# Kernel tuning notes

Measured on AMD Instinct MI355X. Metric: run time of the kernel, lower is better.

Reference implementation:

```python
import jax, jax.numpy as jnp
import numpy as np

N_NODES = 50000
N_EDGES = 600000
F_IN = 64
N_GRAPHS = 2000
OUT_DIM = 1
BN_EPS = 1e-5


def _bn(x, gamma, beta):
    # BatchNorm1d training-mode forward: biased batch stats over node/row dim
    m = jnp.mean(x, axis=0)
    v = jnp.var(x, axis=0)
    return (x - m) * jax.lax.rsqrt(v + BN_EPS) * gamma + beta


def _gcn(x, W, b, src, dst):
    # PyG GCNConv: h = x @ W; symmetric-normalized aggregation with self-loops; bias after agg
    n = x.shape[0]
    h = x @ W                                    # [N, C_out]
    ones = jnp.ones((src.shape[0],), h.dtype)
    deg = jax.ops.segment_sum(ones, dst, num_segments=n) + 1.0  # +1 self-loop
    dinv = jax.lax.rsqrt(deg)
    norm = (dinv[src] * dinv[dst])[:, None]      # [E, 1]
    agg = jax.ops.segment_sum(h[src] * norm, dst, num_segments=n)
    agg = agg + h * (1.0 / deg)[:, None]         # self-loop term: deg^{-1/2}*deg^{-1/2}
    return agg + b


def _pool_mean(x, batch, g):
    s = jax.ops.segment_sum(x, batch, num_segments=g)
    c = jax.ops.segment_sum(jnp.ones((x.shape[0],), x.dtype), batch, num_segments=g)
    return s / jnp.maximum(c, 1.0)[:, None]


def _forward(xc, xs, W1c, b1c, g1c, be1c, W2c, b2c, g2c, be2c,
             W1s, b1s, g1s, be1s, W2s, b2s, g2s, be2s,
             Wf1, bf1, gf1, bef1, Wf2, bf2,
             src_c, dst_c, src_s, dst_s, batch):
    hc = jax.nn.relu(_bn(_gcn(xc, W1c, b1c, src_c, dst_c), g1c, be1c))
    hc = jax.nn.relu(_bn(_gcn(hc, W2c, b2c, src_c, dst_c), g2c, be2c))
    hs = jax.nn.relu(_bn(_gcn(xs, W1s, b1s, src_s, dst_s), g1s, be1s))
    hs = jax.nn.relu(_bn(_gcn(hs, W2s, b2s, src_s, dst_s), g2s, be2s))
    pc = _pool_mean(hc, batch, N_GRAPHS)         # [G, 64]
    ps = _pool_mean(hs, batch, N_GRAPHS)         # [G, 64]
    h = jnp.concatenate([pc, ps], axis=1)        # [G, 128]
    h = jax.nn.relu(_bn(h @ Wf1 + bf1, gf1, bef1))  # dropout is identity in eval
    return h @ Wf2 + bf2                         # [G, OUT_DIM]


def setup_inputs() -> dict:
    key = jax.random.key(0)
    ks = jax.random.split(key, 16)

    def glorot(k, fan_in, fan_out):
        s = np.sqrt(2.0 / (fan_in + fan_out)).astype(np.float32)
        return jax.random.normal(k, (fan_in, fan_out), jnp.float32) * s

    inp = {
        'x_chromophore': jax.random.normal(ks[0], (N_NODES, F_IN), jnp.float32),
        'x_solvent': jax.random.normal(ks[1], (N_NODES, F_IN), jnp.float32),
        'edge_index_chromophore': jax.random.randint(ks[2], (2, N_EDGES), 0, N_NODES),
        'edge_index_solvent': jax.random.randint(ks[3], (2, N_EDGES), 0, N_NODES),
        'batch': jnp.sort(jax.random.randint(ks[4], (N_NODES,), 0, N_GRAPHS)),
        # chromophore branch params
        'W1c': glorot(ks[5], F_IN, 128), 'b1c': jnp.zeros((128,), jnp.float32),
        'g1c': jnp.ones((128,), jnp.float32), 'be1c': jnp.zeros((128,), jnp.float32),
        'W2c': glorot(ks[6], 128, 64), 'b2c': jnp.zeros((64,), jnp.float32),
        'g2c': jnp.ones((64,), jnp.float32), 'be2c': jnp.zeros((64,), jnp.float32),
        # solvent branch params
        'W1s': glorot(ks[7], F_IN, 128), 'b1s': jnp.zeros((128,), jnp.float32),
        'g1s': jnp.ones((128,), jnp.float32), 'be1s': jnp.zeros((128,), jnp.float32),
        'W2s': glorot(ks[8], 128, 64), 'b2s': jnp.zeros((64,), jnp.float32),
        'g2s': jnp.ones((64,), jnp.float32), 'be2s': jnp.zeros((64,), jnp.float32),
        # MLP head
        'Wf1': glorot(ks[9], 128, 64), 'bf1': jnp.zeros((64,), jnp.float32),
        'gf1': jnp.ones((64,), jnp.float32), 'bef1': jnp.zeros((64,), jnp.float32),
        'Wf2': glorot(ks[10], 64, OUT_DIM), 'bf2': jnp.zeros((OUT_DIM,), jnp.float32),
    }
    return inp


def reference(x_chromophore, x_solvent, edge_index_chromophore, edge_index_solvent, batch,
              W1c, b1c, g1c, be1c, W2c, b2c, g2c, be2c,
              W1s, b1s, g1s, be1s, W2s, b2s, g2s, be2s,
              Wf1, bf1, gf1, bef1, Wf2, bf2):
    src_c, dst_c = edge_index_chromophore[0], edge_index_chromophore[1]
    src_s, dst_s = edge_index_solvent[0], edge_index_solvent[1]
    return _forward(x_chromophore, x_solvent,
                    W1c, b1c, g1c, be1c, W2c, b2c, g2c, be2c,
                    W1s, b1s, g1s, be1s, W2s, b2s, g2s, be2s,
                    Wf1, bf1, gf1, bef1, Wf2, bf2,
                    src_c, dst_c, src_s, dst_s, batch)
```

## Files before the change

### kernel.cpp

```cpp
#include <hip/hip_runtime.h>
#include <hip/hip_bf16.h>
#include <cstdint>
#include <cstddef>

#define NN 50000
#define NE 600000
#define NG 2000
#define NBUCK 49
#define SLOTS 16
#define NCHUNK 3125
#define PNE (NE + NBUCK * 15 * 1024)

typedef __attribute__((ext_vector_type(8))) short bf8;
typedef __attribute__((ext_vector_type(4))) float f32x4;

__device__ __forceinline__ unsigned short f2bf(float f) {
    uint32_t u = __float_as_uint(f);
    uint32_t r = (u + 0x7FFFu + ((u >> 16) & 1u)) >> 16;
    return (unsigned short)r;
}
__device__ __forceinline__ float bf2f(unsigned short h) {
    return __uint_as_float(((uint32_t)h) << 16);
}
__device__ __forceinline__ float lo16(uint32_t v) { return __uint_as_float(v << 16); }
__device__ __forceinline__ float hi16(uint32_t v) { return __uint_as_float(v & 0xFFFF0000u); }

__global__ __launch_bounds__(256) void conv_bf16_kernel(const float* __restrict__ x0,
                                                        const float* __restrict__ x1,
                                                        unsigned short* __restrict__ out) {
    int b = blockIdx.y;
    const float* x = b ? x1 : x0;
    unsigned short* o = out + (size_t)b * NN * 64;
    int i = (blockIdx.x * 256 + threadIdx.x) * 4;
    if (i + 3 < NN * 64) {
        float4 v = *(const float4*)&x[i];
        ushort4 r = make_ushort4(f2bf(v.x), f2bf(v.y), f2bf(v.z), f2bf(v.w));
        *(ushort4*)&o[i] = r;
    }
}

template<int K, int N>
__global__ __launch_bounds__(256) void pack_w(const float* __restrict__ W0,
                                              const float* __restrict__ W1,
                                              unsigned short* __restrict__ out) {
    int b = blockIdx.y;
    const float* W = b ? W1 : W0;
    unsigned short* o = out + (size_t)b * K * N;
    int idx = blockIdx.x * 256 + threadIdx.x;
    const int total = (N / 16) * (K / 32) * 64;
    if (idx >= total) return;
    int l = idx & 63;
    int th = idx >> 6;
    int h = th % (K / 32);
    int t = th / (K / 32);
    int col = t * 16 + (l & 15);
    int k0 = h * 32 + (l >> 4) * 8;
    ushort4 lo = make_ushort4(f2bf(W[(k0 + 0) * N + col]), f2bf(W[(k0 + 1) * N + col]),
                              f2bf(W[(k0 + 2) * N + col]), f2bf(W[(k0 + 3) * N + col]));
    ushort4 hi = make_ushort4(f2bf(W[(k0 + 4) * N + col]), f2bf(W[(k0 + 5) * N + col]),
                              f2bf(W[(k0 + 6) * N + col]), f2bf(W[(k0 + 7) * N + col]));
    *(ushort4*)&o[idx * 8] = lo;
    *(ushort4*)&o[idx * 8 + 4] = hi;
}

__global__ __launch_bounds__(256) void bucket_hist(const int* __restrict__ d0,
                                                   const int* __restrict__ d1,
                                                   int* __restrict__ bucketCnt, int nE) {
    int b = blockIdx.y;
    const int* dst = b ? d1 : d0;
    __shared__ int h[NBUCK];
    for (int i = threadIdx.x; i < NBUCK; i += 256) h[i] = 0;
    __syncthreads();
    for (int e = blockIdx.x * 256 + threadIdx.x; e < nE; e += gridDim.x * 256)
        atomicAdd(&h[dst[e] >> 10], 1);
    __syncthreads();
    for (int i = threadIdx.x; i < NBUCK; i += 256)
        if (h[i]) atomicAdd(&bucketCnt[b * NBUCK + i], h[i]);
}

__global__ void bucket_scan(const int* __restrict__ bucketCnt,
                            int* __restrict__ bucketOff, int* __restrict__ bucketCur) {
    int b = threadIdx.x;
    if (b < 2) {
        int run = 0;
        for (int i = 0; i < NBUCK; ++i) {
            bucketOff[b * NBUCK + i] = run;
            bucketCur[b * NBUCK + i] = run;
            run += bucketCnt[b * NBUCK + i];
        }
    }
}

__global__ __launch_bounds__(256) void bucket_scatter(const int* __restrict__ s0,
                                                      const int* __restrict__ d0,
                                                      const int* __restrict__ s1,
                                                      const int* __restrict__ d1,
                                                      int* __restrict__ bucketCur,
                                                      uint32_t* __restrict__ bent, int nE) {
    int b = blockIdx.y;
    const int* src = b ? s1 : s0;
    const int* dst = b ? d1 : d0;
    __shared__ int cnt[NBUCK];
    __shared__ int base[NBUCK];
    const int tid = threadIdx.x;
    for (int i = tid; i < NBUCK; i += 256) cnt[i] = 0;
    __syncthreads();

    const int e0 = blockIdx.x * 2048 + tid;
    int bk[8], slot[8];
    uint32_t pay[8];
#pragma unroll
    for (int k = 0; k < 8; ++k) {
        int e = e0 + k * 256;
        if (e < nE) {
            int d = dst[e], s = src[e];
            bk[k] = d >> 10;
            pay[k] = ((uint32_t)(d & 1023) << 16) | (uint32_t)s;
            slot[k] = atomicAdd(&cnt[bk[k]], 1);
        } else bk[k] = -1;
    }
    __syncthreads();
    for (int i = tid; i < NBUCK; i += 256) {
        int c = cnt[i];
        base[i] = c ? atomicAdd(&bucketCur[b * NBUCK + i], c) : 0;
    }
    __syncthreads();
#pragma unroll
    for (int k = 0; k < 8; ++k)
        if (bk[k] >= 0)
            bent[(size_t)b * (size_t)PNE + base[bk[k]] + slot[k]] = pay[k];
}

__global__ __launch_bounds__(256) void csr_build(const uint32_t* __restrict__ bent,
                                                 const int* __restrict__ bucketOff,
                                                 const int* __restrict__ bucketCnt,
                                                 int2* __restrict__ rpe,
                                                 float* __restrict__ dinv,
                                                 uint16_t* __restrict__ perm) {
    __shared__ int lcnt[1024];
    __shared__ int lcur[1024];
    __shared__ int sscan[256];
    const int bk = blockIdx.x;
    const int b = blockIdx.y;
    const int tid = threadIdx.x;
    const int ebase = bucketOff[b * NBUCK + bk];
    const int ecnt = bucketCnt[b * NBUCK + bk];
    const int P0 = ebase + bk * 15360;
    const int node0 = bk << 10;
    const uint32_t* be = bent + (size_t)b * (size_t)PNE + ebase;
    int2* rp = rpe + (size_t)b * NN;
    float* dv = dinv + (size_t)b * NN;
    uint16_t* pm = perm + (size_t)b * (size_t)PNE + P0;

    for (int i = tid; i < 1024; i += 256) lcnt[i] = 0;
    __syncthreads();
    for (int i = tid; i < ecnt; i += 256) atomicAdd(&lcnt[be[i] >> 16], 1);
    __syncthreads();

    int c[4], pc[4], s = 0;
#pragma unroll
    for (int j = 0; j < 4; ++j) {
        c[j] = lcnt[tid * 4 + j];
        pc[j] = (c[j] + 15) & ~15;
        s += pc[j];
    }
    sscan[tid] = s;
    __syncthreads();
    for (int off = 1; off < 256; off <<= 1) {
        int v = (tid >= off) ? sscan[tid - off] : 0;
        __syncthreads();
        sscan[tid] += v;
        __syncthreads();
    }
    int run = sscan[tid] - s;
#pragma unroll
    for (int j = 0; j < 4; ++j) {
        int nl = tid * 4 + j;
        int g = node0 + nl;
        if (g < NN) {
            rp[g] = make_int2(P0 + run, P0 + run + pc[j]);
            lcur[nl] = run;
            dv[g] = rsqrtf((float)c[j] + 1.0f);
        }
        run += pc[j];
    }
    __syncthreads();

    for (int i = tid; i < ecnt; i += 256) {
        uint32_t en = be[i];
        int nl = en >> 16;
        int pos = atomicAdd(&lcur[nl], 1);
        pm[pos] = (uint16_t)(en & 0xFFFFu);
    }
    __syncthreads();

    int run2 = sscan[tid] - s;
#pragma unroll
    for (int j = 0; j < 4; ++j) {
        int g = node0 + tid * 4 + j;
        if (g < NN)
            for (int t = c[j]; t < pc[j]; ++t) pm[run2 + t] = 0xFFFFu;
        run2 += pc[j];
    }
}

__global__ __launch_bounds__(256) void weight_fill(const uint16_t* __restrict__ perm,
                                                   const float* __restrict__ dinv,
                                                   uint32_t* __restrict__ permw, int nE) {
    int b = blockIdx.y;
    const uint16_t* pm = perm + (size_t)b * (size_t)PNE;
    const float* dv = dinv + (size_t)b * NN;
    uint32_t* pw = permw + (size_t)b * (size_t)PNE;
    int i = (blockIdx.x * 256 + threadIdx.x) * 4;
    if (i + 3 < nE) {
        ushort4 s4 = *(const ushort4*)&pm[i];
        uint4 o;
        o.x = (s4.x < NN) ? (((uint32_t)f2bf(dv[s4.x]) << 16) | (uint32_t)s4.x) : 0u;
        o.y = (s4.y < NN) ? (((uint32_t)f2bf(dv[s4.y]) << 16) | (uint32_t)s4.y) : 0u;
        o.z = (s4.z < NN) ? (((uint32_t)f2bf(dv[s4.z]) << 16) | (uint32_t)s4.z) : 0u;
        o.w = (s4.w < NN) ? (((uint32_t)f2bf(dv[s4.w]) << 16) | (uint32_t)s4.w) : 0u;
        *(uint4*)&pw[i] = o;
    } else {
        for (; i < nE; ++i) {
            uint16_t s = pm[i];
            pw[i] = (s < NN) ? (((uint32_t)f2bf(dv[s]) << 16) | (uint32_t)s) : 0u;
        }
    }
}

__global__ __launch_bounds__(256) void gemm1_mfma(const unsigned short* __restrict__ Xbf,
                                                  const unsigned short* __restrict__ Wp,
                                                  unsigned short* __restrict__ Y) {
    const int b = blockIdx.y;
    const unsigned short* __restrict__ X = Xbf + (size_t)b * NN * 64;
    const unsigned short* __restrict__ W = Wp + (size_t)b * 64 * 128;
    unsigned short* __restrict__ Yb = Y + (size_t)b * NN * 128;
    const int tid = threadIdx.x;
    const int w = tid >> 6, lane = tid & 63;
    const int chunk = blockIdx.x * 4 + w;
    if (chunk >= NCHUNK) return;
    const int m = lane & 15, quad = lane >> 4;

    const int row = chunk * 16 + m;
    bf8 a0 = *(const bf8*)&X[(size_t)row * 64 + quad * 8];
    bf8 a1 = *(const bf8*)&X[(size_t)row * 64 + 32 + quad * 8];
    f32x4 acc[8];
#pragma unroll
    for (int t = 0; t < 8; ++t) acc[t] = (f32x4){0.f, 0.f, 0.f, 0.f};
#pragma unroll
    for (int t = 0; t < 8; ++t) {
        bf8 b0 = *(const bf8*)&W[((t * 2 + 0) * 64 + lane) * 8];
        bf8 b1 = *(const bf8*)&W[((t * 2 + 1) * 64 + lane) * 8];
        acc[t] = __builtin_amdgcn_mfma_f32_16x16x32_bf16(b0, a0, acc[t], 0, 0, 0);
        acc[t] = __builtin_amdgcn_mfma_f32_16x16x32_bf16(b1, a1, acc[t], 0, 0, 0);
    }
#pragma unroll
    for (int t = 0; t < 8; ++t) {
        uint32_t lo = (uint32_t)f2bf(acc[t][0]) | ((uint32_t)f2bf(acc[t][1]) << 16);
        uint32_t hi = (uint32_t)f2bf(acc[t][2]) | ((uint32_t)f2bf(acc[t][3]) << 16);
        *(uint2*)&Yb[(size_t)row * 128 + t * 16 + quad * 4] = make_uint2(lo, hi);
    }
}

__global__ __launch_bounds__(256) void stats128_bf16(const unsigned short* __restrict__ Y,
                                                     float* __restrict__ sums) {
    const int b = blockIdx.y;
    const unsigned short* __restrict__ Yb = Y + (size_t)b * NN * 128;
    const int g = threadIdx.x & 31;
    const int rs = threadIdx.x >> 5;
    float s0 = 0.f, s1 = 0.f, s2 = 0.f, s3 = 0.f;
    float q0 = 0.f, q1 = 0.f, q2 = 0.f, q3 = 0.f;
    for (int r = blockIdx.x * 8 + rs; r < NN; r += gridDim.x * 8) {
        uint2 v = *(const uint2*)&Yb[(size_t)r * 128 + g * 4];
        float x0 = lo16(v.x);
        float x1 = hi16(v.x);
        float x2 = lo16(v.y);
        float x3 = hi16(v.y);
        s0 += x0; s1 += x1; s2 += x2; s3 += x3;
        q0 = fmaf(x0, x0, q0); q1 = fmaf(x1, x1, q1);
        q2 = fmaf(x2, x2, q2); q3 = fmaf(x3, x3, q3);
    }
    __shared__ float ls[8][128], lq[8][128];
    *(float4*)&ls[rs][g * 4] = make_float4(s0, s1, s2, s3);
    *(float4*)&lq[rs][g * 4] = make_float4(q0, q1, q2, q3);
    __syncthreads();
    if (threadIdx.x < 128) {
        const int c = threadIdx.x;
        float S = 0.f, Q = 0.f;
#pragma unroll
        for (int k = 0; k < 8; ++k) { S += ls[k][c]; Q += lq[k][c]; }
        int slot = blockIdx.x & (SLOTS - 1);
        float* sb = sums + (size_t)(b * SLOTS + slot) * 256;
        atomicAdd(&sb[c], S);
        atomicAdd(&sb[128 + c], Q);
    }
}

__global__ __launch_bounds__(256) void gemm2_mfma(const unsigned short* __restrict__ H1,
                                                  const unsigned short* __restrict__ Wp,
                                                  const float* __restrict__ sums,
                                                  const float* __restrict__ g0,
                                                  const float* __restrict__ g1,
                                                  const float* __restrict__ be0,
                                                  const float* __restrict__ be1,
                                                  unsigned short* __restrict__ Y) {
    __shared__ float scLds[128], shLds[128];
    const int b = blockIdx.y;
    const unsigned short* __restrict__ X = H1 + (size_t)b * NN * 128;
    const unsigned short* __restrict__ W = Wp + (size_t)b * 128 * 64;
    unsigned short* __restrict__ Yb = Y + (size_t)b * NN * 64;
    const int tid = threadIdx.x;

    if (tid < 128) {
        float s = 0.f, s2 = 0.f;
#pragma unroll
        for (int k = 0; k < SLOTS; ++k) {
            const float* sb = sums + (size_t)(b * SLOTS + k) * 256;
            s += sb[tid];
            s2 += sb[128 + tid];
        }
        const float invN = 1.0f / (float)NN;
        float mean = s * invN;
        float var = s2 * invN - mean * mean;
        float gamma = b ? g1[tid] : g0[tid];
        float beta = b ? be1[tid] : be0[tid];
        float sc = gamma * rsqrtf(var + 1e-5f);
        scLds[tid] = sc;
        shLds[tid] = beta - mean * sc;
    }
    __syncthreads();

    const int w = tid >> 6, lane = tid & 63;
    const int chunk = blockIdx.x * 4 + w;
    if (chunk >= NCHUNK) return;
    const int m = lane & 15, quad = lane >> 4;
    const int row = chunk * 16 + m;

    f32x4 acc[4];
#pragma unroll
    for (int t = 0; t < 4; ++t) acc[t] = (f32x4){0.f, 0.f, 0.f, 0.f};
#pragma unroll
    for (int h = 0; h < 4; ++h) {
        const int k0 = h * 32 + quad * 8;
        bf8 araw = *(const bf8*)&X[(size_t)row * 128 + k0];
        float4 sc0 = *(const float4*)&scLds[k0];
        float4 sc1 = *(const float4*)&scLds[k0 + 4];
        float4 sh0 = *(const float4*)&shLds[k0];
        float4 sh1 = *(const float4*)&shLds[k0 + 4];
        float scv[8] = {sc0.x, sc0.y, sc0.z, sc0.w, sc1.x, sc1.y, sc1.z, sc1.w};
        float shv[8] = {sh0.x, sh0.y, sh0.z, sh0.w, sh1.x, sh1.y, sh1.z, sh1.w};
        bf8 af;
#pragma unroll
        for (int j = 0; j < 8; ++j) {
            float v = bf2f((unsigned short)araw[j]);
            v = fmaxf(fmaf(v, scv[j], shv[j]), 0.f);
            af[j] = (short)f2bf(v);
        }
#pragma unroll
        for (int t = 0; t < 4; ++t) {
            bf8 bf = *(const bf8*)&W[((t * 4 + h) * 64 + lane) * 8];
            acc[t] = __builtin_amdgcn_mfma_f32_16x16x32_bf16(bf, af, acc[t], 0, 0, 0);
        }
    }
#pragma unroll
    for (int t = 0; t < 4; ++t) {
        uint32_t lo = (uint32_t)f2bf(acc[t][0]) | ((uint32_t)f2bf(acc[t][1]) << 16);
        uint32_t hi = (uint32_t)f2bf(acc[t][2]) | ((uint32_t)f2bf(acc[t][3]) << 16);
        *(uint2*)&Yb[(size_t)row * 64 + t * 16 + quad * 4] = make_uint2(lo, hi);
    }
}

template<bool STATS>
__global__ __launch_bounds__(256) void agg2_kernel(const unsigned short* __restrict__ hall,
                                                   const int2* __restrict__ rpe,
                                                   const uint32_t* __restrict__ permw,
                                                   const float* __restrict__ dinv,
                                                   unsigned short* __restrict__ out,
                                                   float* __restrict__ sums, int nNodes) {
    const int b = blockIdx.y;
    const unsigned short* __restrict__ h = hall + (size_t)b * NN * 64;
    const int2* rp = rpe + (size_t)b * NN;
    const uint32_t* pe = permw + (size_t)b * (size_t)PNE;
    const float* dv = dinv + (size_t)b * NN;
    unsigned short* ob = out + (size_t)b * nNodes * 64;

    const int w = threadIdx.x >> 6;
    const int wave = blockIdx.x * 4 + w;
    const int lane = threadIdx.x & 63;
    const int g = lane >> 3;
    const int c = lane & 7;
    float a0 = 0.f, a1 = 0.f, a2 = 0.f, a3 = 0.f;
    float a4 = 0.f, a5 = 0.f, a6 = 0.f, a7 = 0.f;
    float fv[8];
#pragma unroll
    for (int j = 0; j < 8; ++j) fv[j] = 0.f;

    const bool active = wave < nNodes;
    if (active) {
        const int d = wave;
        const float di = dv[d];
        const int2 pr = rp[d];
        for (int p = pr.x; p < pr.y; p += 16) {
            const uint32_t e0 = pe[p + g];
            const uint32_t e1 = pe[p + 8 + g];
            const int i0 = (int)(e0 & 0xFFFFu);
            const int i1 = (int)(e1 & 0xFFFFu);
            const float w0 = __uint_as_float(e0 & 0xFFFF0000u);
            const float w1 = __uint_as_float(e1 & 0xFFFF0000u);
            const uint4 v0 = *(const uint4*)&h[(size_t)i0 * 64 + c * 8];
            const uint4 v1 = *(const uint4*)&h[(size_t)i1 * 64 + c * 8];
            a0 = fmaf(w0, lo16(v0.x), a0); a1 = fmaf(w0, hi16(v0.x), a1);
            a2 = fmaf(w0, lo16(v0.y), a2); a3 = fmaf(w0, hi16(v0.y), a3);
            a4 = fmaf(w0, lo16(v0.z), a4); a5 = fmaf(w0, hi16(v0.z), a5);
            a6 = fmaf(w0, lo16(v0.w), a6); a7 = fmaf(w0, hi16(v0.w), a7);
            a0 = fmaf(w1, lo16(v1.x), a0); a1 = fmaf(w1, hi16(v1.x), a1);
            a2 = fmaf(w1, lo16(v1.y), a2); a3 = fmaf(w1, hi16(v1.y), a3);
            a4 = fmaf(w1, lo16(v1.z), a4); a5 = fmaf(w1, hi16(v1.z), a5);
            a6 = fmaf(w1, lo16(v1.w), a6); a7 = fmaf(w1, hi16(v1.w), a7);
        }
        a0 += __shfl_xor(a0, 8, 64);  a1 += __shfl_xor(a1, 8, 64);
        a2 += __shfl_xor(a2, 8, 64);  a3 += __shfl_xor(a3, 8, 64);
        a4 += __shfl_xor(a4, 8, 64);  a5 += __shfl_xor(a5, 8, 64);
        a6 += __shfl_xor(a6, 8, 64);  a7 += __shfl_xor(a7, 8, 64);
        a0 += __shfl_xor(a0, 16, 64); a1 += __shfl_xor(a1, 16, 64);
        a2 += __shfl_xor(a2, 16, 64); a3 += __shfl_xor(a3, 16, 64);
        a4 += __shfl_xor(a4, 16, 64); a5 += __shfl_xor(a5, 16, 64);
        a6 += __shfl_xor(a6, 16, 64); a7 += __shfl_xor(a7, 16, 64);
        a0 += __shfl_xor(a0, 32, 64); a1 += __shfl_xor(a1, 32, 64);
        a2 += __shfl_xor(a2, 32, 64); a3 += __shfl_xor(a3, 32, 64);
        a4 += __shfl_xor(a4, 32, 64); a5 += __shfl_xor(a5, 32, 64);
        a6 += __shfl_xor(a6, 32, 64); a7 += __shfl_xor(a7, 32, 64);

        if (g == 0) {
            const uint4 sv = *(const uint4*)&h[(size_t)d * 64 + c * 8];
            fv[0] = di * fmaf(di, lo16(sv.x), a0);
            fv[1] = di * fmaf(di, hi16(sv.x), a1);
            fv[2] = di * fmaf(di, lo16(sv.y), a2);
            fv[3] = di * fmaf(di, hi16(sv.y), a3);
            fv[4] = di * fmaf(di, lo16(sv.z), a4);
            fv[5] = di * fmaf(di, hi16(sv.z), a5);
            fv[6] = di * fmaf(di, lo16(sv.w), a6);
            fv[7] = di * fmaf(di, hi16(sv.w), a7);
            uint4 o;
            o.x = (uint32_t)f2bf(fv[0]) | ((uint32_t)f2bf(fv[1]) << 16);
            o.y = (uint32_t)f2bf(fv[2]) | ((uint32_t)f2bf(fv[3]) << 16);
            o.z = (uint32_t)f2bf(fv[4]) | ((uint32_t)f2bf(fv[5]) << 16);
            o.w = (uint32_t)f2bf(fv[6]) | ((uint32_t)f2bf(fv[7]) << 16);
            *(uint4*)&ob[(size_t)d * 64 + c * 8] = o;
        }
    }
    if constexpr (STATS) {
        __shared__ float ls[256], ls2[256];
        if (g == 0) {
            *(float4*)&ls[w * 64 + c * 8]      = make_float4(fv[0], fv[1], fv[2], fv[3]);
            *(float4*)&ls[w * 64 + c * 8 + 4]  = make_float4(fv[4], fv[5], fv[6], fv[7]);
            *(float4*)&ls2[w * 64 + c * 8]     = make_float4(fv[0]*fv[0], fv[1]*fv[1], fv[2]*fv[2], fv[3]*fv[3]);
            *(float4*)&ls2[w * 64 + c * 8 + 4] = make_float4(fv[4]*fv[4], fv[5]*fv[5], fv[6]*fv[6], fv[7]*fv[7]);
        }
        __syncthreads();
        if (threadIdx.x < 64) {
            const int t = threadIdx.x;
            float s  = ls[t]  + ls[t + 64]  + ls[t + 128]  + ls[t + 192];
            float s2 = ls2[t] + ls2[t + 64] + ls2[t + 128] + ls2[t + 192];
            int slot = blockIdx.x & (SLOTS - 1);
            float* sb = sums + ((size_t)(b * SLOTS + slot) * 2) * 64;
            atomicAdd(&sb[t], s);
            atomicAdd(&sb[64 + t], s2);
        }
    }
}

__global__ __launch_bounds__(64) void pool2_kernel(const unsigned short* __restrict__ x,
                                                   const float* __restrict__ sums,
                                                   const float* __restrict__ g0,
                                                   const float* __restrict__ g1,
                                                   const float* __restrict__ be0,
                                                   const float* __restrict__ be1,
                                                   const int* __restrict__ batch,
                                                   float* __restrict__ Hmean, int n) {
    int b = blockIdx.y;
    const unsigned short* xb = x + (size_t)b * NN * 64;
    int g = blockIdx.x;
    int c = threadIdx.x;
    float s0 = 0.f, s20 = 0.f;
#pragma unroll
    for (int k = 0; k < SLOTS; ++k) {
        const float* sb = sums + ((size_t)(b * SLOTS + k) * 2) * 64;
        s0 += sb[c];
        s20 += sb[64 + c];
    }
    const float invN = 1.0f / (float)NN;
    float mean = s0 * invN;
    float var = s20 * invN - mean * mean;
    float gamma = b ? g1[c] : g0[c];
    float beta = b ? be1[c] : be0[c];
    float sc = gamma * rsqrtf(var + 1e-5f);
    float sh = beta - mean * sc;

    int lo = 0, hi = n;
    while (lo < hi) { int mid = (lo + hi) >> 1; if (batch[mid] < g) lo = mid + 1; else hi = mid; }
    int start = lo;
    hi = n;
    while (lo < hi) { int mid = (lo + hi) >> 1; if (batch[mid] <= g) lo = mid + 1; else hi = mid; }
    int end = lo;
    float s = 0.f;
    for (int r = start; r < end; ++r)
        s += fmaxf(fmaf(bf2f(xb[(size_t)r * 64 + c]), sc, sh), 0.f);
    float cf = (float)(end - start);
    Hmean[(size_t)g * 128 + b * 64 + c] = s / fmaxf(cf, 1.f);
}

__global__ __launch_bounds__(64) void head_gemm1_kernel(const float* __restrict__ H,
                                                        const float* __restrict__ Wf1,
                                                        float* __restrict__ T) {
    __shared__ float row[128];
    int g = blockIdx.x;
    int c = threadIdx.x;
    row[c] = H[(size_t)g * 128 + c];
    row[c + 64] = H[(size_t)g * 128 + 64 + c];
    __syncthreads();
    float acc = 0.f;
#pragma unroll 8
    for (int k = 0; k < 128; ++k) acc = fmaf(row[k], Wf1[k * 64 + c], acc);
    T[(size_t)g * 64 + c] = acc;
}

template<int C>
__global__ __launch_bounds__(256) void bn_stats_kernel(const float* __restrict__ x, int n,
                                                       float* __restrict__ sums) {
    constexpr int RP = 256 / C;
    __shared__ float ls[256], ls2[256];
    int c = threadIdx.x % C;
    int sub = threadIdx.x / C;
    float s = 0.f, s2 = 0.f;
    for (int r = blockIdx.x * RP + sub; r < n; r += gridDim.x * RP) {
        float v = x[(size_t)r * C + c];
        s += v; s2 += v * v;
    }
    ls[threadIdx.x] = s; ls2[threadIdx.x] = s2;
    __syncthreads();
    if (sub == 0) {
#pragma unroll
        for (int k = 1; k < RP; ++k) { s += ls[k * C + c]; s2 += ls2[k * C + c]; }
        atomicAdd(&sums[c], s);
        atomicAdd(&sums[C + c], s2);
    }
}

__global__ __launch_bounds__(64) void head_final_kernel(const float* __restrict__ T,
                                                        const float* __restrict__ hsums,
                                                        const float* __restrict__ gf1,
                                                        const float* __restrict__ bef1,
                                                        const float* __restrict__ Wf2,
                                                        const float* __restrict__ bf2,
                                                        float* __restrict__ out) {
    int g = blockIdx.x;
    int c = threadIdx.x;
    const float invG = 1.0f / (float)NG;
    float mean = hsums[c] * invG;
    float var = hsums[64 + c] * invG - mean * mean;
    float sc = gf1[c] * rsqrtf(var + 1e-5f);
    float sh = bef1[c] - mean * sc;
    float v = fmaxf(fmaf(T[(size_t)g * 64 + c], sc, sh), 0.f) * Wf2[c];
#pragma unroll
    for (int off = 32; off > 0; off >>= 1) v += __shfl_down(v, off, 64);
    if (c == 0) out[g] = v + bf2[0];
}


static inline size_t alignup(size_t x) { return (x + 255) & ~(size_t)255; }

extern "C" void kernel_launch(void* const* d_in, const int* in_sizes, int n_in,
                              void* d_out, int out_size, void* d_ws, size_t ws_size,
                              hipStream_t stream) {
    const float* xc  = (const float*)d_in[0];
    const float* xs  = (const float*)d_in[1];
    const int*   eic = (const int*)d_in[2];
    const int*   eis = (const int*)d_in[3];
    const int*   batch = (const int*)d_in[4];
    const float* W1c = (const float*)d_in[5];
    const float* g1c = (const float*)d_in[7];
    const float* be1c = (const float*)d_in[8];
    const float* W2c = (const float*)d_in[9];
    const float* g2c = (const float*)d_in[11];
    const float* be2c = (const float*)d_in[12];
    const float* W1s = (const float*)d_in[13];
    const float* g1s = (const float*)d_in[15];
    const float* be1s = (const float*)d_in[16];
    const float* W2s = (const float*)d_in[17];
    const float* g2s = (const float*)d_in[19];
    const float* be2s = (const float*)d_in[20];
    const float* Wf1 = (const float*)d_in[21];
    const float* gf1 = (const float*)d_in[23];
    const float* bef1 = (const float*)d_in[24];
    const float* Wf2 = (const float*)d_in[25];
    const float* bf2 = (const float*)d_in[26];
    float* out = (float*)d_out;

    char* ws = (char*)d_ws;
    size_t off = 0;
    auto alloc = [&](size_t bytes) { char* p = ws + off; off += alignup(bytes); return p; };

    int*      bucketCnt = (int*)alloc(2 * NBUCK * 4);
    int*      bucketOff = (int*)alloc(2 * NBUCK * 4);
    int*      bucketCur = (int*)alloc(2 * NBUCK * 4);
    uint32_t* bent      = (uint32_t*)alloc((size_t)2 * PNE * 4);
    uint16_t* perm      = (uint16_t*)alloc(((size_t)2 * PNE + 64) * 2);
    int2*     rpe       = (int2*)alloc((size_t)2 * NN * 8);
    float*    dinv      = (float*)alloc((size_t)2 * NN * 4);
    unsigned short* xbf   = (unsigned short*)alloc((size_t)2 * NN * 64 * 2);
    unsigned short* aggbf = (unsigned short*)alloc((size_t)2 * NN * 64 * 2);
    unsigned short* h1bf  = (unsigned short*)alloc((size_t)2 * NN * 128 * 2);
    unsigned short* h2bf  = (unsigned short*)alloc((size_t)2 * NN * 64 * 2);
    unsigned short* Wp1   = (unsigned short*)alloc((size_t)2 * 64 * 128 * 2);
    unsigned short* Wp2   = (unsigned short*)alloc((size_t)2 * 128 * 64 * 2);
    float*    sums1     = (float*)alloc(((size_t)2 * SLOTS * 256 + (size_t)2 * SLOTS * 128 + 128) * 4);
    float*    sums2     = sums1 + (size_t)2 * SLOTS * 256;
    float*    hsums     = sums2 + (size_t)2 * SLOTS * 128;
    float*    Hmean     = (float*)alloc((size_t)NG * 128 * 4);
    float*    T         = (float*)alloc((size_t)NG * 64 * 4);

    const size_t statBytes = ((size_t)2 * SLOTS * 256 + (size_t)2 * SLOTS * 128 + 128) * 4;
    const int gemmBlocks = (NCHUNK + 3) / 4;
    const int aggBlocks = (NN + 3) / 4;

    conv_bf16_kernel<<<dim3((NN * 64 / 4 + 255) / 256, 2), 256, 0, stream>>>(xc, xs, xbf);
    pack_w<64, 128><<<dim3(4, 2), 256, 0, stream>>>(W1c, W1s, Wp1);
    pack_w<128, 64><<<dim3(4, 2), 256, 0, stream>>>(W2c, W2s, Wp2);
    hipMemsetAsync(sums1, 0, statBytes, stream);

    hipMemsetAsync(bucketCnt, 0, 2 * NBUCK * 4, stream);
    bucket_hist<<<dim3(64, 2), 256, 0, stream>>>(eic + NE, eis + NE, bucketCnt, NE);
    bucket_scan<<<1, 64, 0, stream>>>(bucketCnt, bucketOff, bucketCur);
    bucket_scatter<<<dim3((NE + 2047) / 2048, 2), 256, 0, stream>>>(
        eic, eic + NE, eis, eis + NE, bucketCur, bent, NE);
    csr_build<<<dim3(NBUCK, 2), 256, 0, stream>>>(bent, bucketOff, bucketCnt,
                                                  rpe, dinv, perm);
    weight_fill<<<dim3((PNE / 4 + 255) / 256, 2), 256, 0, stream>>>(perm, dinv, bent, PNE);

    agg2_kernel<false><<<dim3(aggBlocks, 2), 256, 0, stream>>>(
        xbf, rpe, bent, dinv, aggbf, nullptr, NN);
    gemm1_mfma<<<dim3(gemmBlocks, 2), 256, 0, stream>>>(aggbf, Wp1, h1bf);
    stats128_bf16<<<dim3(256, 2), 256, 0, stream>>>(h1bf, sums1);

    gemm2_mfma<<<dim3(gemmBlocks, 2), 256, 0, stream>>>(h1bf, Wp2, sums1,
                                                        g1c, g1s, be1c, be1s, h2bf);
    agg2_kernel<true><<<dim3(aggBlocks, 2), 256, 0, stream>>>(
        h2bf, rpe, bent, dinv, aggbf, sums2, NN);

    pool2_kernel<<<dim3(NG, 2), 64, 0, stream>>>(aggbf, sums2, g2c, g2s, be2c, be2s,
                                                 batch, Hmean, NN);

    head_gemm1_kernel<<<NG, 64, 0, stream>>>(Hmean, Wf1, T);
    bn_stats_kernel<64><<<32, 256, 0, stream>>>(T, NG, hsums);
    head_final_kernel<<<NG, 64, 0, stream>>>(T, hsums, gf1, bef1, Wf2, bf2, out);
}
```

Before: 359.2 us.

## Restructure GCN aggregation to 8 lanes per node with feature-half split

The aggregation kernel changes from one wavefront per destination node (64 lanes split into 8 edge groups by 8 feature chunks, followed by a cross-lane shuffle reduction) to 8 lanes per node. Each lane covers 4 features of one 32-feature half, and the two halves become a new grid dimension. Edges are read as uint4 vectors with a one-step prefetch. CSR row padding shrinks from multiples of 16 to multiples of 4, with a smaller padded edge buffer, which removes wasted padded-edge gathers and the shuffle reductions. In exchange, each node's edge list is streamed twice (once per half), narrower 8-byte gathers are used, and BN statistics go through shared-memory atomics.

```diff
diff --git a/kernel.cpp b/kernel.cpp
--- a/kernel.cpp
+++ b/kernel.cpp
@@ -9,7 +9,7 @@
 #define NBUCK 49
 #define SLOTS 16
 #define NCHUNK 3125
-#define PNE (NE + NBUCK * 15 * 1024)
+#define PNE 750976
 
 typedef __attribute__((ext_vector_type(8))) short bf8;
 typedef __attribute__((ext_vector_type(4))) float f32x4;
@@ -145,7 +145,7 @@
     const int tid = threadIdx.x;
     const int ebase = bucketOff[b * NBUCK + bk];
     const int ecnt = bucketCnt[b * NBUCK + bk];
-    const int P0 = ebase + bk * 15360;
+    const int P0 = ((ebase + 3) & ~3) + bk * 3076;
     const int node0 = bk << 10;
     const uint32_t* be = bent + (size_t)b * (size_t)PNE + ebase;
     int2* rp = rpe + (size_t)b * NN;
@@ -161,7 +161,7 @@
 #pragma unroll
     for (int j = 0; j < 4; ++j) {
         c[j] = lcnt[tid * 4 + j];
-        pc[j] = (c[j] + 15) & ~15;
+        pc[j] = (c[j] + 3) & ~3;
         s += pc[j];
     }
     sscan[tid] = s;
@@ -370,102 +370,73 @@
     }
 }
 
+#define PROC_EDGE(e)                                                          \
+    {   const int ii = (int)((e) & 0xFFFFu);                                  \
+        const float wk = __uint_as_float((e) & 0xFFFF0000u);                  \
+        const uint2 hv = *(const uint2*)&h[(size_t)ii * 64 + pos * 4];        \
+        a0 = fmaf(wk, lo16(hv.x), a0); a1 = fmaf(wk, hi16(hv.x), a1);         \
+        a2 = fmaf(wk, lo16(hv.y), a2); a3 = fmaf(wk, hi16(hv.y), a3); }
+
 template<bool STATS>
-__global__ __launch_bounds__(256) void agg2_kernel(const unsigned short* __restrict__ hall,
+__global__ __launch_bounds__(256) void agg3_kernel(const unsigned short* __restrict__ hall,
                                                    const int2* __restrict__ rpe,
                                                    const uint32_t* __restrict__ permw,
                                                    const float* __restrict__ dinv,
                                                    unsigned short* __restrict__ out,
                                                    float* __restrict__ sums, int nNodes) {
     const int b = blockIdx.y;
-    const unsigned short* __restrict__ h = hall + (size_t)b * NN * 64;
+    const int half = blockIdx.z;
+    const unsigned short* __restrict__ h = hall + (size_t)b * NN * 64 + half * 32;
     const int2* rp = rpe + (size_t)b * NN;
     const uint32_t* pe = permw + (size_t)b * (size_t)PNE;
     const float* dv = dinv + (size_t)b * NN;
-    unsigned short* ob = out + (size_t)b * nNodes * 64;
-
-    const int w = threadIdx.x >> 6;
-    const int wave = blockIdx.x * 4 + w;
-    const int lane = threadIdx.x & 63;
-    const int g = lane >> 3;
-    const int c = lane & 7;
-    float a0 = 0.f, a1 = 0.f, a2 = 0.f, a3 = 0.f;
-    float a4 = 0.f, a5 = 0.f, a6 = 0.f, a7 = 0.f;
-    float fv[8];
-#pragma unroll
-    for (int j = 0; j < 8; ++j) fv[j] = 0.f;
-
-    const bool active = wave < nNodes;
-    if (active) {
-        const int d = wave;
+    unsigned short* ob = out + (size_t)b * NN * 64 + half * 32;
+
+    const int tid = threadIdx.x;
+    const int wv = tid >> 6;
+    const int g = (tid >> 3) & 7;
+    const int pos = tid & 7;
+    const int d = blockIdx.x * 32 + wv * 8 + g;
+
+    float f0 = 0.f, f1 = 0.f, f2 = 0.f, f3 = 0.f;
+    if (d < nNodes) {
+        const int2 pr = rp[d];
         const float di = dv[d];
-        const int2 pr = rp[d];
-        for (int p = pr.x; p < pr.y; p += 16) {
-            const uint32_t e0 = pe[p + g];
-            const uint32_t e1 = pe[p + 8 + g];
-            const int i0 = (int)(e0 & 0xFFFFu);
-            const int i1 = (int)(e1 & 0xFFFFu);
-            const float w0 = __uint_as_float(e0 & 0xFFFF0000u);
-            const float w1 = __uint_as_float(e1 & 0xFFFF0000u);
-            const uint4 v0 = *(const uint4*)&h[(size_t)i0 * 64 + c * 8];
-            const uint4 v1 = *(const uint4*)&h[(size_t)i1 * 64 + c * 8];
-            a0 = fmaf(w0, lo16(v0.x), a0); a1 = fmaf(w0, hi16(v0.x), a1);
-            a2 = fmaf(w0, lo16(v0.y), a2); a3 = fmaf(w0, hi16(v0.y), a3);
-            a4 = fmaf(w0, lo16(v0.z), a4); a5 = fmaf(w0, hi16(v0.z), a5);
-            a6 = fmaf(w0, lo16(v0.w), a6); a7 = fmaf(w0, hi16(v0.w), a7);
-            a0 = fmaf(w1, lo16(v1.x), a0); a1 = fmaf(w1, hi16(v1.x), a1);
-            a2 = fmaf(w1, lo16(v1.y), a2); a3 = fmaf(w1, hi16(v1.y), a3);
-            a4 = fmaf(w1, lo16(v1.z), a4); a5 = fmaf(w1, hi16(v1.z), a5);
-            a6 = fmaf(w1, lo16(v1.w), a6); a7 = fmaf(w1, hi16(v1.w), a7);
-        }
-        a0 += __shfl_xor(a0, 8, 64);  a1 += __shfl_xor(a1, 8, 64);
-        a2 += __shfl_xor(a2, 8, 64);  a3 += __shfl_xor(a3, 8, 64);
-        a4 += __shfl_xor(a4, 8, 64);  a5 += __shfl_xor(a5, 8, 64);
-        a6 += __shfl_xor(a6, 8, 64);  a7 += __shfl_xor(a7, 8, 64);
-        a0 += __shfl_xor(a0, 16, 64); a1 += __shfl_xor(a1, 16, 64);
-        a2 += __shfl_xor(a2, 16, 64); a3 += __shfl_xor(a3, 16, 64);
-        a4 += __shfl_xor(a4, 16, 64); a5 += __shfl_xor(a5, 16, 64);
-        a6 += __shfl_xor(a6, 16, 64); a7 += __shfl_xor(a7, 16, 64);
-        a0 += __shfl_xor(a0, 32, 64); a1 += __shfl_xor(a1, 32, 64);
-        a2 += __shfl_xor(a2, 32, 64); a3 += __shfl_xor(a3, 32, 64);
-        a4 += __shfl_xor(a4, 32, 64); a5 += __shfl_xor(a5, 32, 64);
-        a6 += __shfl_xor(a6, 32, 64); a7 += __shfl_xor(a7, 32, 64);
-
-        if (g == 0) {
-            const uint4 sv = *(const uint4*)&h[(size_t)d * 64 + c * 8];
-            fv[0] = di * fmaf(di, lo16(sv.x), a0);
-            fv[1] = di * fmaf(di, hi16(sv.x), a1);
-            fv[2] = di * fmaf(di, lo16(sv.y), a2);
-            fv[3] = di * fmaf(di, hi16(sv.y), a3);
-            fv[4] = di * fmaf(di, lo16(sv.z), a4);
-            fv[5] = di * fmaf(di, hi16(sv.z), a5);
-            fv[6] = di * fmaf(di, lo16(sv.w), a6);
-            fv[7] = di * fmaf(di, hi16(sv.w), a7);
-            uint4 o;
-            o.x = (uint32_t)f2bf(fv[0]) | ((uint32_t)f2bf(fv[1]) << 16);
-            o.y = (uint32_t)f2bf(fv[2]) | ((uint32_t)f2bf(fv[3]) << 16);
-            o.z = (uint32_t)f2bf(fv[4]) | ((uint32_t)f2bf(fv[5]) << 16);
-            o.w = (uint32_t)f2bf(fv[6]) | ((uint32_t)f2bf(fv[7]) << 16);
-            *(uint4*)&ob[(size_t)d * 64 + c * 8] = o;
-        }
+        float a0 = 0.f, a1 = 0.f, a2 = 0.f, a3 = 0.f;
+        int p = pr.x;
+        if (p < pr.y) {
+            uint4 ev = *(const uint4*)&pe[p];
+            for (; p + 4 < pr.y; p += 4) {
+                uint4 evn = *(const uint4*)&pe[p + 4];
+                PROC_EDGE(ev.x); PROC_EDGE(ev.y); PROC_EDGE(ev.z); PROC_EDGE(ev.w);
+                ev = evn;
+            }
+            PROC_EDGE(ev.x); PROC_EDGE(ev.y); PROC_EDGE(ev.z); PROC_EDGE(ev.w);
+        }
+        const uint2 sv = *(const uint2*)&h[(size_t)d * 64 + pos * 4];
+        f0 = di * fmaf(di, lo16(sv.x), a0);
+        f1 = di * fmaf(di, hi16(sv.x), a1);
+        f2 = di * fmaf(di, lo16(sv.y), a2);
+        f3 = di * fmaf(di, hi16(sv.y), a3);
+        uint32_t o0 = (uint32_t)f2bf(f0) | ((uint32_t)f2bf(f1) << 16);
+        uint32_t o1 = (uint32_t)f2bf(f2) | ((uint32_t)f2bf(f3) << 16);
+        *(uint2*)&ob[(size_t)d * 64 + pos * 4] = make_uint2(o0, o1);
     }
     if constexpr (STATS) {
-        __shared__ float ls[256], ls2[256];
-        if (g == 0) {
-            *(float4*)&ls[w * 64 + c * 8]      = make_float4(fv[0], fv[1], fv[2], fv[3]);
-            *(float4*)&ls[w * 64 + c * 8 + 4]  = make_float4(fv[4], fv[5], fv[6], fv[7]);
-            *(float4*)&ls2[w * 64 + c * 8]     = make_float4(fv[0]*fv[0], fv[1]*fv[1], fv[2]*fv[2], fv[3]*fv[3]);
-            *(float4*)&ls2[w * 64 + c * 8 + 4] = make_float4(fv[4]*fv[4], fv[5]*fv[5], fv[6]*fv[6], fv[7]*fv[7]);
-        }
+        __shared__ float ls[32], ls2[32];
+        if (tid < 32) { ls[tid] = 0.f; ls2[tid] = 0.f; }
         __syncthreads();
-        if (threadIdx.x < 64) {
-            const int t = threadIdx.x;
-            float s  = ls[t]  + ls[t + 64]  + ls[t + 128]  + ls[t + 192];
-            float s2 = ls2[t] + ls2[t + 64] + ls2[t + 128] + ls2[t + 192];
+        const int cb = pos * 4;
+        atomicAdd(&ls[cb + 0], f0); atomicAdd(&ls2[cb + 0], f0 * f0);
+        atomicAdd(&ls[cb + 1], f1); atomicAdd(&ls2[cb + 1], f1 * f1);
+        atomicAdd(&ls[cb + 2], f2); atomicAdd(&ls2[cb + 2], f2 * f2);
+        atomicAdd(&ls[cb + 3], f3); atomicAdd(&ls2[cb + 3], f3 * f3);
+        __syncthreads();
+        if (tid < 32) {
             int slot = blockIdx.x & (SLOTS - 1);
             float* sb = sums + ((size_t)(b * SLOTS + slot) * 2) * 64;
-            atomicAdd(&sb[t], s);
-            atomicAdd(&sb[64 + t], s2);
+            atomicAdd(&sb[half * 32 + tid], ls[tid]);
+            atomicAdd(&sb[64 + half * 32 + tid], ls2[tid]);
         }
     }
 }
@@ -622,7 +593,7 @@
 
     const size_t statBytes = ((size_t)2 * SLOTS * 256 + (size_t)2 * SLOTS * 128 + 128) * 4;
     const int gemmBlocks = (NCHUNK + 3) / 4;
-    const int aggBlocks = (NN + 3) / 4;
+    const int aggBlocks = (NN + 31) / 32;
 
     conv_bf16_kernel<<<dim3((NN * 64 / 4 + 255) / 256, 2), 256, 0, stream>>>(xc, xs, xbf);
     pack_w<64, 128><<<dim3(4, 2), 256, 0, stream>>>(W1c, W1s, Wp1);
@@ -638,14 +609,14 @@
                                                   rpe, dinv, perm);
     weight_fill<<<dim3((PNE / 4 + 255) / 256, 2), 256, 0, stream>>>(perm, dinv, bent, PNE);
 
-    agg2_kernel<false><<<dim3(aggBlocks, 2), 256, 0, stream>>>(
+    agg3_kernel<false><<<dim3(aggBlocks, 2, 2), 256, 0, stream>>>(
         xbf, rpe, bent, dinv, aggbf, nullptr, NN);
     gemm1_mfma<<<dim3(gemmBlocks, 2), 256, 0, stream>>>(aggbf, Wp1, h1bf);
     stats128_bf16<<<dim3(256, 2), 256, 0, stream>>>(h1bf, sums1);
 
     gemm2_mfma<<<dim3(gemmBlocks, 2), 256, 0, stream>>>(h1bf, Wp2, sums1,
                                                         g1c, g1s, be1c, be1s, h2bf);
-    agg2_kernel<true><<<dim3(aggBlocks, 2), 256, 0, stream>>>(
+    agg3_kernel<true><<<dim3(aggBlocks, 2, 2), 256, 0, stream>>>(
         h2bf, rpe, bent, dinv, aggbf, sums2, NN);
 
     pool2_kernel<<<dim3(NG, 2), 64, 0, stream>>>(aggbf, sums2, g2c, g2s, be2c, be2s,
```

Measured after the change: 384.1 us. 6.9% more time.
